# Performance work log

Hardware: AMD Instinct MI355X
Metric: run time of the kernel (lower is better)

Reference implementation:

```python
import jax, jax.numpy as jnp
import numpy as np

B, H, W, C, NC = 4, 64, 64, 64, 19


def setup_inputs() -> dict:
    key = jax.random.key(0)
    ks = jax.random.split(key, 12)
    s = 0.05  # small init so sigmoid scores are not saturated
    return {
        "feature": jax.random.normal(ks[0], (B, H, W, C), dtype=jnp.float32),
        "predict": jax.random.normal(ks[1], (B, H, W, NC), dtype=jnp.float32),
        # height attention params (dim = H); k_linear in source is unused (q reused as k)
        "hq_w": jax.random.normal(ks[2], (H, H), dtype=jnp.float32) * s,
        "hq_b": jnp.zeros((H,), dtype=jnp.float32),
        "hv_w": jax.random.normal(ks[3], (H, H), dtype=jnp.float32) * s,
        "hv_b": jnp.zeros((H,), dtype=jnp.float32),
        # width attention params (dim = W)
        "wq_w": jax.random.normal(ks[4], (W, W), dtype=jnp.float32) * s,
        "wq_b": jnp.zeros((W,), dtype=jnp.float32),
        "wv_w": jax.random.normal(ks[5], (W, W), dtype=jnp.float32) * s,
        "wv_b": jnp.zeros((W,), dtype=jnp.float32),
        # gating scalars (nn.Parameter(torch.zeros(1)) in source; random here to exercise path)
        "h_gate": jax.random.normal(ks[6], (1,), dtype=jnp.float32) * 0.5,
        "w_gate": jax.random.normal(ks[7], (1,), dtype=jnp.float32) * 0.5,
        # 1x1 conv num_classes -> 1 (stored as [NC, 1] matrix; 1x1 conv == per-pixel linear)
        "conv_w": jax.random.normal(ks[8], (NC, 1), dtype=jnp.float32) * s,
        "conv_b": jnp.zeros((1,), dtype=jnp.float32),
    }


def _self_atten(x, wq, bq, wv, bv, dim):
    # Source uses q_linear for BOTH q and k (k_linear dead), softmax replaced by sigmoid.
    q = x @ wq + bq                                   # [B, N, dim]
    v = x @ wv + bv                                   # [B, N, dim]
    scores = jax.nn.sigmoid(jnp.einsum('bnd,bmd->bnm', q, q) / jnp.sqrt(jnp.float32(dim)))
    return jnp.einsum('bnm,bmd->bnd', scores, v)      # [B, N, dim]


def _axial(x, hq_w, hq_b, hv_w, hv_b, wq_w, wq_b, wv_w, wv_b, h_gate, w_gate):
    b, h, w, c = x.shape
    # height attention: seq = W*C, feature dim = H
    xh = x.transpose(0, 2, 3, 1).reshape(b, w * c, h)
    xh = _self_atten(xh, hq_w, hq_b, hv_w, hv_b, h)
    xh = xh.reshape(b, w, c, h).transpose(0, 3, 1, 2)  # back to [B,H,W,C]
    x = xh * h_gate + x
    # width attention: seq = H*C, feature dim = W
    xw = x.transpose(0, 1, 3, 2).reshape(b, h * c, w)
    xw = _self_atten(xw, wq_w, wq_b, wv_w, wv_b, w)
    xw = xw.reshape(b, h, c, w).transpose(0, 1, 3, 2)  # back to [B,H,W,C]
    x = xw * w_gate + x
    return x


def reference(feature, predict, hq_w, hq_b, hv_w, hv_b, wq_w, wq_b, wv_w, wv_b,
              h_gate, w_gate, conv_w, conv_b):
    feat = feature + _axial(feature, hq_w, hq_b, hv_w, hv_b,
                            wq_w, wq_b, wv_w, wv_b, h_gate, w_gate)
    p = 1.0 - jax.nn.sigmoid(predict)                 # [B,H,W,NC]
    p = p @ conv_w + conv_b                           # 1x1 conv -> [B,H,W,1]
    return p * feat                                   # broadcast gate -> [B,H,W,C]
```

## Files before the change

kernel.cpp:

```cpp
#include <hip/hip_runtime.h>

typedef short bf16x8 __attribute__((ext_vector_type(8)));
typedef float f32x16 __attribute__((ext_vector_type(16)));

__device__ __forceinline__ unsigned short f2bf(float f) {
    union { float f; unsigned int u; } v; v.f = f;
    unsigned int r = v.u + 0x7fffu + ((v.u >> 16) & 1u);
    return (unsigned short)(r >> 16);
}

__device__ __forceinline__ unsigned int pack_bf16(float a, float b) {
#if __has_builtin(__builtin_amdgcn_cvt_pk_bf16_f32)
    typedef __bf16 bf16x2 __attribute__((ext_vector_type(2)));
    bf16x2 p = __builtin_amdgcn_cvt_pk_bf16_f32(a, b);
    union { bf16x2 v; unsigned int u; } c; c.v = p;
    return c.u;
#else
    return (unsigned int)f2bf(a) | ((unsigned int)f2bf(b) << 16);
#endif
}

__device__ __forceinline__ float fast_sigmoid8(float x) {
    float e = __builtin_exp2f(x * -0.180336880f);
    return __builtin_amdgcn_rcpf(1.0f + e);
}

__global__ __launch_bounds__(256) void prep_kernel(
    const float* __restrict__ src,
    const float* __restrict__ wq, const float* __restrict__ bq,
    const float* __restrict__ wv, const float* __restrict__ bv,
    unsigned short* __restrict__ Qg, unsigned short* __restrict__ Vtg)
{
    __shared__ float slab[64][65];
    __shared__ float wqs[4096];
    __shared__ float wvs[4096];

    const int t  = threadIdx.x;
    const int bx = blockIdx.x, b = blockIdx.y;

    {
        const float4* wq4 = (const float4*)wq;
        const float4* wv4 = (const float4*)wv;
        float4* q4 = (float4*)wqs; float4* v4 = (float4*)wvs;
        #pragma unroll
        for (int i = 0; i < 4; ++i) {
            q4[i*256 + t] = wq4[i*256 + t];
            v4[i*256 + t] = wv4[i*256 + t];
        }
    }
    {
        const int k = t >> 2, c0 = (t & 3) << 4;
        const size_t sb = (size_t)b*262144 + (size_t)k*4096 + (size_t)bx*64 + c0;
        #pragma unroll
        for (int i = 0; i < 4; ++i)
            *(float4*)&slab[k][c0 + i*4] = *(const float4*)&src[sb + i*4];
    }
    __syncthreads();

    const int c = t & 63, jg = t >> 6;
    float qa[16], va[16];
    #pragma unroll
    for (int jj = 0; jj < 16; ++jj) { qa[jj] = bq[jg*16+jj]; va[jj] = bv[jg*16+jj]; }
    for (int k = 0; k < 64; ++k) {
        const float xv = slab[k][c];
        const float* wqr = &wqs[k*64 + jg*16];
        const float* wvr = &wvs[k*64 + jg*16];
        #pragma unroll
        for (int jj = 0; jj < 16; ++jj) {
            qa[jj] += xv * wqr[jj];
            va[jj] += xv * wvr[jj];
        }
    }
    const int token = bx*64 + c;
    union { unsigned short s[16]; uint4 v[2]; } qp, vp;
    #pragma unroll
    for (int jj = 0; jj < 16; ++jj) { qp.s[jj] = f2bf(qa[jj]); vp.s[jj] = f2bf(va[jj]); }
    const size_t qoff = ((size_t)b*4096 + token)*64 + jg*16;
    *(uint4*)&Qg[qoff]     = qp.v[0];
    *(uint4*)&Qg[qoff + 8] = qp.v[1];
    #pragma unroll
    for (int jj = 0; jj < 16; ++jj)
        Vtg[((size_t)b*64 + jg*16 + jj)*4096 + token] = vp.s[jj];
}

__global__ __launch_bounds__(256) void prep_w_kernel(
    const float* __restrict__ feature, const float* __restrict__ Pin,
    const float* __restrict__ gate,
    const float* __restrict__ wq, const float* __restrict__ bq,
    const float* __restrict__ wv, const float* __restrict__ bv,
    unsigned short* __restrict__ Qg, unsigned short* __restrict__ Vtg,
    float* __restrict__ x1out, int nsplit)
{
    __shared__ float slab[64][65];
    __shared__ float wqs[4096];
    __shared__ float wvs[4096];

    const int t  = threadIdx.x;
    const int bx = blockIdx.x, b = blockIdx.y;

    {
        const float4* wq4 = (const float4*)wq;
        const float4* wv4 = (const float4*)wv;
        float4* q4 = (float4*)wqs; float4* v4 = (float4*)wvs;
        #pragma unroll
        for (int i = 0; i < 4; ++i) {
            q4[i*256 + t] = wq4[i*256 + t];
            v4[i*256 + t] = wv4[i*256 + t];
        }
    }
    {
        const int k = t >> 2, c0 = (t & 3) << 4;
        const size_t off = (size_t)bx*4096 + (size_t)k*64 + c0;
        const size_t fb  = (size_t)b*262144 + off;
        const float g = gate[0];
        #pragma unroll
        for (int i = 0; i < 4; ++i) {
            float4 v  = *(const float4*)&feature[fb + i*4];
            float sx = 0.f, sy = 0.f, sz = 0.f, sw = 0.f;
            for (int ks = 0; ks < nsplit; ++ks) {
                float4 pk = *(const float4*)&Pin[((size_t)(ks*4 + b) << 18) + off + i*4];
                sx += pk.x; sy += pk.y; sz += pk.z; sw += pk.w;
            }
            v.x += g * sx; v.y += g * sy; v.z += g * sz; v.w += g * sw;
            *(float4*)&slab[k][c0 + i*4] = v;
            *(float4*)&x1out[fb + i*4] = v;
        }
    }
    __syncthreads();

    const int c = t & 63, jg = t >> 6;
    float qa[16], va[16];
    #pragma unroll
    for (int jj = 0; jj < 16; ++jj) { qa[jj] = bq[jg*16+jj]; va[jj] = bv[jg*16+jj]; }
    for (int k = 0; k < 64; ++k) {
        const float xv = slab[k][c];
        const float* wqr = &wqs[k*64 + jg*16];
        const float* wvr = &wvs[k*64 + jg*16];
        #pragma unroll
        for (int jj = 0; jj < 16; ++jj) {
            qa[jj] += xv * wqr[jj];
            va[jj] += xv * wvr[jj];
        }
    }
    const int token = bx*64 + c;
    union { unsigned short s[16]; uint4 v[2]; } qp, vp;
    #pragma unroll
    for (int jj = 0; jj < 16; ++jj) { qp.s[jj] = f2bf(qa[jj]); vp.s[jj] = f2bf(va[jj]); }
    const size_t qoff = ((size_t)b*4096 + token)*64 + jg*16;
    *(uint4*)&Qg[qoff]     = qp.v[0];
    *(uint4*)&Qg[qoff + 8] = qp.v[1];
    #pragma unroll
    for (int jj = 0; jj < 16; ++jj)
        Vtg[((size_t)b*64 + jg*16 + jj)*4096 + token] = vp.s[jj];
}

__global__ __launch_bounds__(256) void attn_kernel(
    const unsigned short* __restrict__ Qg,
    const unsigned short* __restrict__ Vtg,
    float* __restrict__ P)
{
    __shared__ unsigned short Ksh[64][72];
    __shared__ unsigned short Vts[64][72];
    __shared__ unsigned short Ss[128][72];

    const int t = threadIdx.x;
    const int mb = blockIdx.x, b = blockIdx.y, ksplit = blockIdx.z;
    const int nsp = gridDim.z;
    const int niter = 64 / nsp;
    const int keybase = ksplit * (4096 / nsp);
    const int lane = t & 63, w = t >> 6;
    const int l32 = lane & 31, hi = lane >> 5;

    const unsigned short* Qbase = Qg  + (size_t)b*262144;
    const unsigned short* Vbase = Vtg + (size_t)b*262144;

    bf16x8 qb[4];
    {
        const unsigned short* qrow = Qbase + (size_t)(mb*128 + w*32 + l32)*64 + hi*8;
        qb[0] = *(const bf16x8*)(qrow);
        qb[1] = *(const bf16x8*)(qrow + 16);
        qb[2] = *(const bf16x8*)(qrow + 32);
        qb[3] = *(const bf16x8*)(qrow + 48);
    }

    f32x16 y[2];
    #pragma unroll
    for (int i = 0; i < 16; ++i) { y[0][i] = 0.f; y[1][i] = 0.f; }

    const int lrow = t >> 2;
    const int loff = (t & 3) << 4;
    {
        const uint4* gk = (const uint4*)(Qbase + (size_t)(keybase + lrow)*64 + loff);
        uint4 k0 = gk[0], k1 = gk[1];
        const uint4* gv = (const uint4*)(Vbase + (size_t)lrow*4096 + keybase + loff);
        uint4 v0 = gv[0], v1 = gv[1];
        *(uint4*)&Ksh[lrow][loff]     = k0;
        *(uint4*)&Ksh[lrow][loff + 8] = k1;
        *(uint4*)&Vts[lrow][loff]     = v0;
        *(uint4*)&Vts[lrow][loff + 8] = v1;
    }
    __syncthreads();

    unsigned short* srowS = &Ss[w*32 + l32][0];
    unsigned int*   srowU = (unsigned int*)srowS;

    for (int kb = 0; kb < niter; ++kb) {
        uint4 nk0 = {0,0,0,0}, nk1 = {0,0,0,0}, nv0 = {0,0,0,0}, nv1 = {0,0,0,0};
        if (kb < niter - 1) {
            const int keyn = keybase + (kb + 1)*64;
            const uint4* gk = (const uint4*)(Qbase + (size_t)(keyn + lrow)*64 + loff);
            nk0 = gk[0]; nk1 = gk[1];
            const uint4* gv = (const uint4*)(Vbase + (size_t)lrow*4096 + keyn + loff);
            nv0 = gv[0]; nv1 = gv[1];
        }

        f32x16 tt[2];
        #pragma unroll
        for (int i = 0; i < 16; ++i) { tt[0][i] = 0.f; tt[1][i] = 0.f; }
        #pragma unroll
        for (int s = 0; s < 4; ++s) {
            const int co = s*16 + hi*8;
            bf16x8 ka0 = *(const bf16x8*)&Ksh[l32][co];
            bf16x8 ka1 = *(const bf16x8*)&Ksh[32 + l32][co];
            tt[0] = __builtin_amdgcn_mfma_f32_32x32x16_bf16(ka0, qb[s], tt[0], 0,0,0);
            tt[1] = __builtin_amdgcn_mfma_f32_32x32x16_bf16(ka1, qb[s], tt[1], 0,0,0);
        }

        #pragma unroll
        for (int u = 0; u < 2; ++u)
            #pragma unroll
            for (int g = 0; g < 4; ++g) {
                uint2 pk;
                pk.x = pack_bf16(fast_sigmoid8(tt[u][4*g+0]), fast_sigmoid8(tt[u][4*g+1]));
                pk.y = pack_bf16(fast_sigmoid8(tt[u][4*g+2]), fast_sigmoid8(tt[u][4*g+3]));
                *(uint2*)&srowU[u*16 + g*4 + hi*2] = pk;
            }

        #pragma unroll
        for (int ks = 0; ks < 4; ++ks) {
            const int co = ks*16 + hi*8;
            bf16x8 sa  = *(const bf16x8*)&srowS[co];
            bf16x8 vb0 = *(const bf16x8*)&Vts[l32][co];
            bf16x8 vb1 = *(const bf16x8*)&Vts[32 + l32][co];
            y[0] = __builtin_amdgcn_mfma_f32_32x32x16_bf16(sa, vb0, y[0], 0,0,0);
            y[1] = __builtin_amdgcn_mfma_f32_32x32x16_bf16(sa, vb1, y[1], 0,0,0);
        }

        __syncthreads();
        if (kb < niter - 1) {
            *(uint4*)&Ksh[lrow][loff]     = nk0;
            *(uint4*)&Ksh[lrow][loff + 8] = nk1;
            *(uint4*)&Vts[lrow][loff]     = nv0;
            *(uint4*)&Vts[lrow][loff + 8] = nv1;
        }
        __syncthreads();
    }

    float* Pp = P + (((size_t)(ksplit*4 + b)) << 18);
    const int token0 = mb*128 + w*32 + hi*4;
    #pragma unroll
    for (int dt = 0; dt < 2; ++dt) {
        const int d = dt*32 + l32;
        #pragma unroll
        for (int g = 0; g < 4; ++g) {
            float4 v;
            v.x = y[dt][4*g+0]; v.y = y[dt][4*g+1];
            v.z = y[dt][4*g+2]; v.w = y[dt][4*g+3];
            *(float4*)&Pp[(size_t)d*4096 + token0 + 8*g] = v;
        }
    }
}

__global__ __launch_bounds__(256) void final_kernel(
    const float* __restrict__ feature, const float* __restrict__ x1,
    const float* __restrict__ Pin, const float* __restrict__ predict,
    const float* __restrict__ conv_w, const float* __restrict__ conv_b,
    const float* __restrict__ gate, float* __restrict__ out, int nsplit)
{
    const int i4 = blockIdx.x * 256 + threadIdx.x;
    const int j = i4 << 2;
    const int pix = j >> 6;
    const float* row = predict + (size_t)pix * 19;
    float pv = conv_b[0];
    #pragma unroll
    for (int i = 0; i < 19; ++i) {
        float sg = __builtin_amdgcn_rcpf(1.0f + __builtin_exp2f(-1.442695041f * row[i]));
        pv += (1.0f - sg) * conv_w[i];
    }

    const int b = j >> 18, h = (j >> 12) & 63, d = (j >> 6) & 63, c = j & 63;
    const size_t pif = ((size_t)(b*64 + d) << 12) + h*64 + c;
    float sx = 0.f, sy = 0.f, sz = 0.f, sw = 0.f;
    for (int ks = 0; ks < nsplit; ++ks) {
        float4 pk = *(const float4*)&Pin[((size_t)ks << 20) + pif];
        sx += pk.x; sy += pk.y; sz += pk.z; sw += pk.w;
    }
    const float g = gate[0];
    float4 f = ((const float4*)feature)[i4];
    float4 x = ((const float4*)x1)[i4];
    float4 o;
    o.x = pv * (f.x + x.x + g * sx);
    o.y = pv * (f.y + x.y + g * sy);
    o.z = pv * (f.z + x.z + g * sz);
    o.w = pv * (f.w + x.w + g * sw);
    ((float4*)out)[i4] = o;
}

extern "C" void kernel_launch(void* const* d_in, const int* in_sizes, int n_in,
                              void* d_out, int out_size, void* d_ws, size_t ws_size,
                              hipStream_t stream) {
    const float* feature = (const float*)d_in[0];
    const float* predict = (const float*)d_in[1];
    const float* hq_w = (const float*)d_in[2];
    const float* hq_b = (const float*)d_in[3];
    const float* hv_w = (const float*)d_in[4];
    const float* hv_b = (const float*)d_in[5];
    const float* wq_w = (const float*)d_in[6];
    const float* wq_b = (const float*)d_in[7];
    const float* wv_w = (const float*)d_in[8];
    const float* wv_b = (const float*)d_in[9];
    const float* h_gate = (const float*)d_in[10];
    const float* w_gate = (const float*)d_in[11];
    const float* conv_w = (const float*)d_in[12];
    const float* conv_b = (const float*)d_in[13];
    float* out = (float*)d_out;

    char* ws = (char*)d_ws;
    unsigned short* Qg  = (unsigned short*)(ws);
    unsigned short* Vtg = (unsigned short*)(ws + (2u << 20));
    float*          x1  = (float*)(ws + (4u << 20));
    float*          P   = (float*)(ws + (8u << 20));
    const int nsplit = (ws_size >= (40u << 20)) ? 8 : 4;

    dim3 blk(256);
    prep_kernel<<<dim3(64, 4), blk, 0, stream>>>(feature, hq_w, hq_b, hv_w, hv_b,
                                                 Qg, Vtg);
    attn_kernel<<<dim3(32, 4, nsplit), blk, 0, stream>>>(Qg, Vtg, P);
    prep_w_kernel<<<dim3(64, 4), blk, 0, stream>>>(feature, P, h_gate,
                                                   wq_w, wq_b, wv_w, wv_b,
                                                   Qg, Vtg, x1, nsplit);
    attn_kernel<<<dim3(32, 4, nsplit), blk, 0, stream>>>(Qg, Vtg, P);
    final_kernel<<<dim3(1024), blk, 0, stream>>>(feature, x1, P, predict,
                                                 conv_w, conv_b, w_gate, out, nsplit);
}
```

Before: 215.8 us.

## Switch attention to fp16 MFMA and pass sigmoid scores through registers

Moves Q/V storage and both attention MFMAs from bf16 to fp16, with packed round-toward-zero conversion. The sigmoid scale is folded into the Q fragment once, so each score needs only exp2 and rcp. The score matrix no longer round-trips through shared memory: lanes swap packed halves with cross-lane shuffles to build the A operand of the second MFMA directly, which removes the Ss buffer and its LDS traffic. The key split is fixed at 4, halving the partial buffers for the final reduction at the cost of less grid parallelism. Fp16 has a narrower range than bf16, which could matter if activations grow large.

```diff
diff --git a/kernel.cpp b/kernel.cpp
--- a/kernel.cpp
+++ b/kernel.cpp
@@ -1,28 +1,21 @@
 #include <hip/hip_runtime.h>
 
-typedef short bf16x8 __attribute__((ext_vector_type(8)));
+typedef _Float16 f16x8 __attribute__((ext_vector_type(8)));
+typedef __fp16   fp16x2 __attribute__((ext_vector_type(2)));
 typedef float f32x16 __attribute__((ext_vector_type(16)));
 
-__device__ __forceinline__ unsigned short f2bf(float f) {
-    union { float f; unsigned int u; } v; v.f = f;
-    unsigned int r = v.u + 0x7fffu + ((v.u >> 16) & 1u);
-    return (unsigned short)(r >> 16);
-}
-
-__device__ __forceinline__ unsigned int pack_bf16(float a, float b) {
-#if __has_builtin(__builtin_amdgcn_cvt_pk_bf16_f32)
-    typedef __bf16 bf16x2 __attribute__((ext_vector_type(2)));
-    bf16x2 p = __builtin_amdgcn_cvt_pk_bf16_f32(a, b);
-    union { bf16x2 v; unsigned int u; } c; c.v = p;
-    return c.u;
-#else
-    return (unsigned int)f2bf(a) | ((unsigned int)f2bf(b) << 16);
-#endif
-}
-
-__device__ __forceinline__ float fast_sigmoid8(float x) {
-    float e = __builtin_exp2f(x * -0.180336880f);
-    return __builtin_amdgcn_rcpf(1.0f + e);
+__device__ __forceinline__ unsigned pkrtz(float a, float b) {
+    fp16x2 h = __builtin_amdgcn_cvt_pkrtz(a, b);
+    union { fp16x2 h; unsigned u; } c; c.h = h; return c.u;
+}
+
+__device__ __forceinline__ unsigned short f2h(float f) {
+    _Float16 h = (_Float16)f;
+    union { _Float16 h; unsigned short s; } c; c.h = h; return c.s;
+}
+
+__device__ __forceinline__ float sig_from_t(float t) {
+    return __builtin_amdgcn_rcpf(1.0f + __builtin_exp2f(t));
 }
 
 __global__ __launch_bounds__(256) void prep_kernel(
@@ -72,15 +65,15 @@
         }
     }
     const int token = bx*64 + c;
-    union { unsigned short s[16]; uint4 v[2]; } qp, vp;
-    #pragma unroll
-    for (int jj = 0; jj < 16; ++jj) { qp.s[jj] = f2bf(qa[jj]); vp.s[jj] = f2bf(va[jj]); }
+    union { unsigned u[8]; uint4 v[2]; } qp;
+    #pragma unroll
+    for (int jj = 0; jj < 8; ++jj) qp.u[jj] = pkrtz(qa[2*jj], qa[2*jj+1]);
     const size_t qoff = ((size_t)b*4096 + token)*64 + jg*16;
     *(uint4*)&Qg[qoff]     = qp.v[0];
     *(uint4*)&Qg[qoff + 8] = qp.v[1];
     #pragma unroll
     for (int jj = 0; jj < 16; ++jj)
-        Vtg[((size_t)b*64 + jg*16 + jj)*4096 + token] = vp.s[jj];
+        Vtg[((size_t)b*64 + jg*16 + jj)*4096 + token] = f2h(va[jj]);
 }
 
 __global__ __launch_bounds__(256) void prep_w_kernel(
@@ -143,15 +136,15 @@
         }
     }
     const int token = bx*64 + c;
-    union { unsigned short s[16]; uint4 v[2]; } qp, vp;
-    #pragma unroll
-    for (int jj = 0; jj < 16; ++jj) { qp.s[jj] = f2bf(qa[jj]); vp.s[jj] = f2bf(va[jj]); }
+    union { unsigned u[8]; uint4 v[2]; } qp;
+    #pragma unroll
+    for (int jj = 0; jj < 8; ++jj) qp.u[jj] = pkrtz(qa[2*jj], qa[2*jj+1]);
     const size_t qoff = ((size_t)b*4096 + token)*64 + jg*16;
     *(uint4*)&Qg[qoff]     = qp.v[0];
     *(uint4*)&Qg[qoff + 8] = qp.v[1];
     #pragma unroll
     for (int jj = 0; jj < 16; ++jj)
-        Vtg[((size_t)b*64 + jg*16 + jj)*4096 + token] = vp.s[jj];
+        Vtg[((size_t)b*64 + jg*16 + jj)*4096 + token] = f2h(va[jj]);
 }
 
 __global__ __launch_bounds__(256) void attn_kernel(
@@ -161,7 +154,6 @@
 {
     __shared__ unsigned short Ksh[64][72];
     __shared__ unsigned short Vts[64][72];
-    __shared__ unsigned short Ss[128][72];
 
     const int t = threadIdx.x;
     const int mb = blockIdx.x, b = blockIdx.y, ksplit = blockIdx.z;
@@ -174,13 +166,15 @@
     const unsigned short* Qbase = Qg  + (size_t)b*262144;
     const unsigned short* Vbase = Vtg + (size_t)b*262144;
 
-    bf16x8 qb[4];
+    f16x8 qb[4];
     {
         const unsigned short* qrow = Qbase + (size_t)(mb*128 + w*32 + l32)*64 + hi*8;
-        qb[0] = *(const bf16x8*)(qrow);
-        qb[1] = *(const bf16x8*)(qrow + 16);
-        qb[2] = *(const bf16x8*)(qrow + 32);
-        qb[3] = *(const bf16x8*)(qrow + 48);
+        const _Float16 sc = (_Float16)(-0.180336880f);
+        #pragma unroll
+        for (int s = 0; s < 4; ++s) {
+            f16x8 q = *(const f16x8*)(qrow + s*16);
+            qb[s] = q * sc;
+        }
     }
 
     f32x16 y[2];
@@ -201,9 +195,6 @@
     }
     __syncthreads();
 
-    unsigned short* srowS = &Ss[w*32 + l32][0];
-    unsigned int*   srowU = (unsigned int*)srowS;
-
     for (int kb = 0; kb < niter; ++kb) {
         uint4 nk0 = {0,0,0,0}, nk1 = {0,0,0,0}, nv0 = {0,0,0,0}, nv1 = {0,0,0,0};
         if (kb < niter - 1) {
@@ -220,30 +211,41 @@
         #pragma unroll
         for (int s = 0; s < 4; ++s) {
             const int co = s*16 + hi*8;
-            bf16x8 ka0 = *(const bf16x8*)&Ksh[l32][co];
-            bf16x8 ka1 = *(const bf16x8*)&Ksh[32 + l32][co];
-            tt[0] = __builtin_amdgcn_mfma_f32_32x32x16_bf16(ka0, qb[s], tt[0], 0,0,0);
-            tt[1] = __builtin_amdgcn_mfma_f32_32x32x16_bf16(ka1, qb[s], tt[1], 0,0,0);
-        }
-
-        #pragma unroll
-        for (int u = 0; u < 2; ++u)
+            f16x8 ka0 = *(const f16x8*)&Ksh[l32][co];
+            f16x8 ka1 = *(const f16x8*)&Ksh[32 + l32][co];
+            tt[0] = __builtin_amdgcn_mfma_f32_32x32x16_f16(ka0, qb[s], tt[0], 0,0,0);
+            tt[1] = __builtin_amdgcn_mfma_f32_32x32x16_f16(ka1, qb[s], tt[1], 0,0,0);
+        }
+
+        #pragma unroll
+        for (int u = 0; u < 2; ++u) {
+            float sg[16];
             #pragma unroll
-            for (int g = 0; g < 4; ++g) {
-                uint2 pk;
-                pk.x = pack_bf16(fast_sigmoid8(tt[u][4*g+0]), fast_sigmoid8(tt[u][4*g+1]));
-                pk.y = pack_bf16(fast_sigmoid8(tt[u][4*g+2]), fast_sigmoid8(tt[u][4*g+3]));
-                *(uint2*)&srowU[u*16 + g*4 + hi*2] = pk;
+            for (int r = 0; r < 16; ++r) sg[r] = sig_from_t(tt[u][r]);
+            #pragma unroll
+            for (int ksh = 0; ksh < 2; ++ksh) {
+                const int bR = ksh*8;
+                unsigned Pa = pkrtz(sg[bR+0], sg[bR+1]);
+                unsigned Pb = pkrtz(sg[bR+2], sg[bR+3]);
+                unsigned Qa = pkrtz(sg[bR+4], sg[bR+5]);
+                unsigned Qb = pkrtz(sg[bR+6], sg[bR+7]);
+                unsigned xPa = __shfl_xor(Pa, 32);
+                unsigned xPb = __shfl_xor(Pb, 32);
+                unsigned xQa = __shfl_xor(Qa, 32);
+                unsigned xQb = __shfl_xor(Qb, 32);
+                union { unsigned u[4]; f16x8 v; } sa;
+                sa.u[0] = hi ? xQa : Pa;
+                sa.u[1] = hi ? xQb : Pb;
+                sa.u[2] = hi ? Qa : xPa;
+                sa.u[3] = hi ? Qb : xPb;
+
+                const int ks = u*2 + ksh;
+                const int co = ks*16 + hi*8;
+                f16x8 vb0 = *(const f16x8*)&Vts[l32][co];
+                f16x8 vb1 = *(const f16x8*)&Vts[32 + l32][co];
+                y[0] = __builtin_amdgcn_mfma_f32_32x32x16_f16(sa.v, vb0, y[0], 0,0,0);
+                y[1] = __builtin_amdgcn_mfma_f32_32x32x16_f16(sa.v, vb1, y[1], 0,0,0);
             }
-
-        #pragma unroll
-        for (int ks = 0; ks < 4; ++ks) {
-            const int co = ks*16 + hi*8;
-            bf16x8 sa  = *(const bf16x8*)&srowS[co];
-            bf16x8 vb0 = *(const bf16x8*)&Vts[l32][co];
-            bf16x8 vb1 = *(const bf16x8*)&Vts[32 + l32][co];
-            y[0] = __builtin_amdgcn_mfma_f32_32x32x16_bf16(sa, vb0, y[0], 0,0,0);
-            y[1] = __builtin_amdgcn_mfma_f32_32x32x16_bf16(sa, vb1, y[1], 0,0,0);
         }
 
         __syncthreads();
@@ -330,7 +332,7 @@
     unsigned short* Vtg = (unsigned short*)(ws + (2u << 20));
     float*          x1  = (float*)(ws + (4u << 20));
     float*          P   = (float*)(ws + (8u << 20));
-    const int nsplit = (ws_size >= (40u << 20)) ? 8 : 4;
+    const int nsplit = 4;
 
     dim3 blk(256);
     prep_kernel<<<dim3(64, 4), blk, 0, stream>>>(feature, hq_w, hq_b, hv_w, hv_b,
```

After: 189.2 us. -12.3%, faster.
